# Optimization experiments

Measured on AMD Instinct MI355X. Metric: run time of the kernel, lower is better.

The kernel has to match this reference:

```python
import jax, jax.numpy as jnp
import numpy as np

KEY_DIM = 32
VALUE_DIM = 64
HEADS = 8
CHAN = 256


def conv1x1(x, w, b):
    # x: [b, c, h, w], w: [out, c], b: [out]  (1x1 conv == channel matmul)
    return jnp.einsum('bchw,oc->bohw', x, w) + b[None, :, None, None]


def setup_inputs() -> dict:
    key = jax.random.key(0)
    ks = jax.random.split(key, 9)
    b, c, h, w = 8, CHAN, 128, 128
    qk_dim = KEY_DIM * HEADS   # 256
    v_dim = VALUE_DIM * HEADS  # 512
    s = 0.02
    return {
        'x':  jax.random.normal(ks[0], (b, c, h, w), jnp.float32),
        'Wq': jax.random.normal(ks[1], (qk_dim, c), jnp.float32) * s,
        'bq': jnp.zeros((qk_dim,), jnp.float32),
        'Wk': jax.random.normal(ks[2], (qk_dim, c), jnp.float32) * s,
        'bk': jnp.zeros((qk_dim,), jnp.float32),
        'Wv': jax.random.normal(ks[3], (v_dim, c), jnp.float32) * s,
        'bv': jnp.zeros((v_dim,), jnp.float32),
        'Wo': jax.random.normal(ks[4], (c, v_dim), jnp.float32) * s,
        'bo': jnp.zeros((c,), jnp.float32),
    }


def reference(x, Wq, bq, Wk, bk, Wv, bv, Wo, bo):
    b, c, h, w = x.shape
    n = h * w
    scale = KEY_DIM ** (-0.25)
    # 1x1 conv projections, reshape to [b, heads, d, n]
    q = conv1x1(x, Wq, bq).reshape(b, HEADS, KEY_DIM, n) * scale
    k = conv1x1(x, Wk, bk).reshape(b, HEADS, KEY_DIM, n) * scale
    v = conv1x1(x, Wv, bv).reshape(b, HEADS, VALUE_DIM, n)
    # softmax over sequence positions for keys
    k = jax.nn.softmax(k, axis=-1)
    # norm_queries=True: softmax over key dim for queries
    q = jax.nn.softmax(q, axis=-2)
    # linear attention: context [b,h,d_k,d_v], then output [b,h,d_v,n]
    ctx = jnp.einsum('bhdn,bhen->bhde', k, v)
    out = jnp.einsum('bhdn,bhde->bhen', q, ctx)
    out = out.reshape(b, HEADS * VALUE_DIM, h, w)
    return conv1x1(out, Wo, bo)
```

## Files before the change

### kernel.cpp

```cpp
#include <hip/hip_runtime.h>
#include <hip/hip_bf16.h>
#include <cstddef>


constexpr int   NPIX     = 16384;
constexpr float QK_SCALE = 0.42044820762685725f;

typedef __attribute__((ext_vector_type(8))) short          bf16x8;
typedef __attribute__((ext_vector_type(8))) unsigned short u16x8;
typedef __attribute__((ext_vector_type(4))) float          f32x4;

__device__ __forceinline__ float bf2f(unsigned short v) {
    union { unsigned int u; float f; } c; c.u = ((unsigned int)v) << 16; return c.f;
}
__device__ __forceinline__ unsigned short f2bf(float f) {
    union { __hip_bfloat16 h; unsigned short s; } c; c.h = __float2bfloat16(f); return c.s;
}
__device__ __forceinline__ void gload_lds16(const void* g, void* l) {
    __builtin_amdgcn_global_load_lds(
        (const __attribute__((address_space(1))) unsigned int*)g,
        (__attribute__((address_space(3))) unsigned int*)l, 16, 0, 0);
}

typedef unsigned short lds_row32[32];

__global__ __launch_bounds__(256) void prep(
    const float* __restrict__ Wq, const float* __restrict__ Wk,
    unsigned short* __restrict__ Wqb, unsigned short* __restrict__ Wkb)
{
    const int i = blockIdx.x * 256 + threadIdx.x;
    Wqb[i] = f2bf(Wq[i]);
    Wkb[i] = f2bf(Wk[i]);
}

template<bool QPASS>
__global__ __launch_bounds__(256) void proj_mfma(
    const float* __restrict__ x, const unsigned short* __restrict__ Wb,
    const float* __restrict__ bias, unsigned short* __restrict__ eout,
    float* __restrict__ ksump2)
{
    __shared__ alignas(16) unsigned char smem[36864];
    lds_row32* As1 = (lds_row32*)smem;
    unsigned short (*BsT)[40] = (unsigned short(*)[40])(smem + 16384);
    const int b  = blockIdx.z;
    const int m0 = blockIdx.y * 128;
    const int n0 = blockIdx.x * 128;
    const int t  = threadIdx.x;
    const int w  = t >> 6, l = t & 63;
    const int lm = l & 15, lg = l >> 4;
    const int mwl = (w & 1) * 64;
    const int nwl = (w >> 1) * 64;
    const int lgs = (lg ^ ((lm & 3) ^ ((lm >> 2) & 3))) * 8;
    const int r16 = l >> 2;
    const int scb = ((l & 3) ^ ((r16 & 3) ^ ((r16 >> 2) & 3))) * 8;

    const unsigned short* Abase = Wb + (size_t)m0 * 256;
    const float* xb = x + (size_t)b * 256 * NPIX + n0;
    const int np = (t & 63) * 2, kq = (t >> 6) * 8;

    f32x4 acc[4][4] = {};
    for (int k0 = 0; k0 < 256; k0 += 32) {
        #pragma unroll
        for (int i = 0; i < 2; ++i) {
            const int row0 = w*32 + i*16;
            gload_lds16(Abase + (size_t)(row0 + r16)*256 + k0 + scb, &As1[row0][0]);
        }
        {
            const float* src = xb + (size_t)(k0 + kq) * NPIX + np;
            float2 v[8];
            #pragma unroll
            for (int r = 0; r < 8; ++r)
                v[r] = *(const float2*)(src + (size_t)r * NPIX);
            u16x8 pa, pb;
            #pragma unroll
            for (int r = 0; r < 8; ++r) { pa[r] = f2bf(v[r].x); pb[r] = f2bf(v[r].y); }
            *(u16x8*)&BsT[np][kq]     = pa;
            *(u16x8*)&BsT[np + 1][kq] = pb;
        }
        __syncthreads();
        bf16x8 afr[4], bfr[4];
        #pragma unroll
        for (int i = 0; i < 4; ++i)
            afr[i] = *(const bf16x8*)&As1[mwl + i*16 + lm][lgs];
        #pragma unroll
        for (int j = 0; j < 4; ++j)
            bfr[j] = *(const bf16x8*)&BsT[nwl + j*16 + lm][lg*8];
        #pragma unroll
        for (int i = 0; i < 4; ++i)
            #pragma unroll
            for (int j = 0; j < 4; ++j)
                acc[i][j] = __builtin_amdgcn_mfma_f32_16x16x32_bf16(afr[i], bfr[j], acc[i][j], 0, 0, 0);
        __syncthreads();
    }

    unsigned short (*Cs)[64][72] = (unsigned short(*)[64][72])smem;
    const int mw = m0 + mwl, nw = n0 + nwl;
    float ksloc[4][4];
    #pragma unroll
    for (int i = 0; i < 4; ++i) {
        const f32x4 bb4 = *(const f32x4*)(bias + mw + i*16 + lg*4);
        #pragma unroll
        for (int r = 0; r < 4; ++r) {
            const int row = i*16 + lg*4 + r;
            float cs = 0.f;
            #pragma unroll
            for (int j = 0; j < 4; ++j) {
                const int col = j*16 + lm;
                const unsigned short bs = f2bf(__expf(QK_SCALE * (acc[i][j][r] + bb4[r])));
                if (QPASS) Cs[w][col][row] = bs;
                else { Cs[w][row][col] = bs; cs += bf2f(bs); }
            }
            ksloc[i][r] = cs;
        }
    }
    if (!QPASS) {
        #pragma unroll
        for (int i = 0; i < 4; ++i)
            #pragma unroll
            for (int r = 0; r < 4; ++r) {
                float v = ksloc[i][r];
                v += __shfl_xor(v, 1, 64);
                v += __shfl_xor(v, 2, 64);
                v += __shfl_xor(v, 4, 64);
                v += __shfl_xor(v, 8, 64);
                if (lm == 0) {
                    const int nt2 = blockIdx.x * 2 + (w >> 1);
                    ksump2[((size_t)b*256 + nt2)*256 + mw + i*16 + lg*4 + r] = v;
                }
            }
    }
    __syncthreads();

    if (QPASS) {
        unsigned short* dst = eout + ((size_t)b * NPIX + nw + l) * 256 + mw;
        u16x8 vv[8];
        float z0 = 0.f, z1 = 0.f;
        #pragma unroll
        for (int s8 = 0; s8 < 8; ++s8) {
            vv[s8] = *(const u16x8*)&Cs[w][l][s8*8];
            float ps = 0.f;
            #pragma unroll
            for (int u = 0; u < 8; ++u) ps += bf2f(vv[s8][u]);
            if (s8 < 4) z0 += ps; else z1 += ps;
        }
        const float iz0 = 1.0f / z0, iz1 = 1.0f / z1;
        #pragma unroll
        for (int s8 = 0; s8 < 8; ++s8) {
            const float iz = (s8 < 4) ? iz0 : iz1;
            u16x8 o;
            #pragma unroll
            for (int u = 0; u < 8; ++u) o[u] = f2bf(bf2f(vv[s8][u]) * iz);
            *(u16x8*)(dst + s8*8) = o;
        }
    } else {
        unsigned short* dst = eout + ((size_t)b * 256 + mw + l) * NPIX + nw;
        #pragma unroll
        for (int s8 = 0; s8 < 8; ++s8)
            *(u16x8*)(dst + s8*8) = *(const u16x8*)&Cs[w][l][s8*8];
    }
}

__global__ __launch_bounds__(256) void ksum_red(
    const float* __restrict__ ksump2, float* __restrict__ ksum)
{
    const int t = threadIdx.x;
    const int row = blockIdx.x * 32 + (t >> 3);
    const int b = row >> 8, c = row & 255;
    const int nt0 = t & 7;
    float s = 0.f;
    #pragma unroll 8
    for (int i = 0; i < 32; ++i)
        s += ksump2[((size_t)b*256 + nt0 + 8*i)*256 + c];
    s += __shfl_xor(s, 1, 64);
    s += __shfl_xor(s, 2, 64);
    s += __shfl_xor(s, 4, 64);
    if (nt0 == 0) ksum[row] = s;
}

template<int NCH>
__global__ __launch_bounds__(256) void t_mfma(
    const unsigned short* __restrict__ ek, const float* __restrict__ x,
    float* __restrict__ Tpart)
{
    __shared__ alignas(16) unsigned char smem[32768];
    lds_row32* As = (lds_row32*)smem;
    lds_row32* Bs = (lds_row32*)(smem + 16384);
    const int bid  = blockIdx.x;
    const int v    = bid & 7, s = bid >> 3;
    const int gidx = s >> 2, q = s & 3;
    const int group = v + 8 * gidx;
    const int b = group / NCH, chunk = group % NCH;
    const int mt = (q >> 1) * 128, ct = (q & 1) * 128;
    constexpr int CHPX = NPIX / NCH;

    const int t = threadIdx.x;
    const int w = t >> 6, l = t & 63;
    const int lm = l & 15, lg = l >> 4;
    const int mw = (w & 1) * 64, cw = (w >> 1) * 64;
    const int r16 = l >> 2;
    const int scb = ((l & 3) ^ ((r16 & 3) ^ ((r16 >> 2) & 3))) * 8;
    const int lgs = (lg ^ ((lm & 3) ^ ((lm >> 2) & 3))) * 8;
    const int brq = t >> 3;
    const int bc4 = (t & 7) * 4;
    const int bslot = (t & 7) >> 1;
    const int bhalf = (t & 1) * 4;

    const unsigned short* Abase = ek + ((size_t)b*256 + mt) * NPIX;
    const float*          Bbase = x  + ((size_t)b*256 + ct) * NPIX;
    const int p0base = chunk * CHPX;

    f32x4 breg[4];
    f32x4 acc[4][4] = {};

    #pragma unroll
    for (int i = 0; i < 2; ++i) {
        const int row0 = w*32 + i*16;
        gload_lds16(Abase + (size_t)(row0 + r16) * NPIX + p0base + scb, &As[row0][0]);
    }
    #pragma unroll
    for (int it = 0; it < 4; ++it)
        breg[it] = *(const f32x4*)(Bbase + (size_t)(it*32 + brq) * NPIX + p0base + bc4);
    #pragma unroll
    for (int it = 0; it < 4; ++it) {
        const int row = it*32 + brq;
        const int sl = bslot ^ ((row & 3) ^ ((row >> 2) & 3));
        unsigned short o[4] = { f2bf(breg[it].x), f2bf(breg[it].y),
                                f2bf(breg[it].z), f2bf(breg[it].w) };
        *(ushort4*)&Bs[row][sl*8 + bhalf] = *(ushort4*)o;
    }
    __syncthreads();

    constexpr int ITERS = CHPX / 32;
    for (int t8 = 0; t8 < ITERS; ++t8) {
        const int cur = t8 & 1;
        if (t8 < ITERS - 1) {
            const int p0 = p0base + (t8 + 1) * 32;
            #pragma unroll
            for (int i = 0; i < 2; ++i) {
                const int row0 = w*32 + i*16;
                gload_lds16(Abase + (size_t)(row0 + r16) * NPIX + p0 + scb,
                            &As[(cur^1)*128 + row0][0]);
            }
            #pragma unroll
            for (int it = 0; it < 4; ++it)
                breg[it] = *(const f32x4*)(Bbase + (size_t)(it*32 + brq) * NPIX + p0 + bc4);
        }
        bf16x8 afr[4], bfr[4];
        #pragma unroll
        for (int i = 0; i < 4; ++i)
            afr[i] = *(const bf16x8*)&As[cur*128 + mw + i*16 + lm][lgs];
        #pragma unroll
        for (int j = 0; j < 4; ++j)
            bfr[j] = *(const bf16x8*)&Bs[cur*128 + cw + j*16 + lm][lgs];
        #pragma unroll
        for (int i = 0; i < 4; ++i)
            #pragma unroll
            for (int j = 0; j < 4; ++j)
                acc[i][j] = __builtin_amdgcn_mfma_f32_16x16x32_bf16(afr[i], bfr[j], acc[i][j], 0, 0, 0);
        if (t8 < ITERS - 1) {
            #pragma unroll
            for (int it = 0; it < 4; ++it) {
                const int row = it*32 + brq;
                const int sl = bslot ^ ((row & 3) ^ ((row >> 2) & 3));
                unsigned short o[4] = { f2bf(breg[it].x), f2bf(breg[it].y),
                                        f2bf(breg[it].z), f2bf(breg[it].w) };
                *(ushort4*)&Bs[(cur^1)*128 + row][sl*8 + bhalf] = *(ushort4*)o;
            }
        }
        __syncthreads();
    }

    float* dst = Tpart + ((size_t)(b*NCH + chunk) * 256) * 256;
    #pragma unroll
    for (int i = 0; i < 4; ++i)
        #pragma unroll
        for (int r = 0; r < 4; ++r) {
            const int gm = mt + mw + i*16 + lg*4 + r;
            #pragma unroll
            for (int j = 0; j < 4; ++j)
                dst[(size_t)gm * 256 + ct + cw + j*16 + lm] = acc[i][j][r];
        }
}

template<int NCH>
__global__ __launch_bounds__(256) void treduce(
    float* __restrict__ Tpart, const float* __restrict__ ksum)
{
    const int gid = blockIdx.x * 256 + threadIdx.x;
    const int b   = gid >> 14;
    const int rem = gid & 16383;
    const int r   = rem >> 6;
    const int c4  = (rem & 63) * 4;
    float* base = Tpart + (((size_t)b*NCH) * 256 + r) * 256 + c4;
    f32x4 s = *(f32x4*)base;
    #pragma unroll
    for (int ch = 1; ch < NCH; ++ch) {
        f32x4 v = *(const f32x4*)(base + (size_t)ch * 65536);
        s.x += v.x; s.y += v.y; s.z += v.z; s.w += v.w;
    }
    const float inv = 1.0f / ksum[b*256 + r];
    s.x *= inv; s.y *= inv; s.z *= inv; s.w *= inv;
    *(f32x4*)base = s;
}

template<int NCH>
__global__ __launch_bounds__(256) void ctx_pass(
    const float* __restrict__ Tpart, const float* __restrict__ Wv,
    const float* __restrict__ bv, float* __restrict__ ctx)
{
    const int gid = blockIdx.x * 256 + threadIdx.x;
    const int b   = gid >> 14;
    const int rem = gid & 16383;
    const int h   = rem >> 11;
    const int de  = rem & 2047;
    const int d   = de >> 6;
    const int e   = de & 63;
    const float* tp = Tpart + (((size_t)b*NCH) * 256 + h*32 + d) * 256;
    const float* wv = Wv + (size_t)(h*64 + e) * 256;
    float sx = 0.f, sy = 0.f, sz = 0.f, sw = 0.f;
    #pragma unroll 8
    for (int c = 0; c < 256; c += 4) {
        f32x4 a = *(const f32x4*)(tp + c);
        f32x4 wv4 = *(const f32x4*)(wv + c);
        sx = fmaf(a.x, wv4.x, sx); sy = fmaf(a.y, wv4.y, sy);
        sz = fmaf(a.z, wv4.z, sz); sw = fmaf(a.w, wv4.w, sw);
    }
    ctx[gid] = (sx + sy) + (sz + sw) + bv[h*64 + e];
}

__global__ __launch_bounds__(256) void mpass(
    const float* __restrict__ ctx, const float* __restrict__ Wo,
    unsigned short* __restrict__ Mb)
{
    const int gid = blockIdx.x * 256 + threadIdx.x;
    const int b   = gid >> 16;
    const int rem = gid & 65535;
    const int o   = rem >> 8;
    const int dg  = rem & 255;
    const int h   = dg >> 5;
    const float* cp = ctx + ((size_t)b*8 + h) * 2048 + (dg & 31) * 64;
    const float* wp = Wo + (size_t)o * 512 + h*64;
    float sx = 0.f, sy = 0.f, sz = 0.f, sw = 0.f;
    #pragma unroll
    for (int e = 0; e < 64; e += 4) {
        f32x4 a = *(const f32x4*)(cp + e);
        f32x4 wv = *(const f32x4*)(wp + e);
        sx = fmaf(a.x, wv.x, sx); sy = fmaf(a.y, wv.y, sy);
        sz = fmaf(a.z, wv.z, sz); sw = fmaf(a.w, wv.w, sw);
    }
    Mb[((size_t)b*256 + o) * 256 + dg] = f2bf((sx + sy) + (sz + sw));
}

__global__ __launch_bounds__(256) void out_mfma(
    const unsigned short* __restrict__ eqT, const unsigned short* __restrict__ Mb,
    const float* __restrict__ bo, float* __restrict__ out)
{
    __shared__ alignas(16) unsigned char smem[32768];
    lds_row32* As0 = (lds_row32*)smem;
    lds_row32* Bs0 = (lds_row32*)(smem + 16384);
    const int b  = blockIdx.z;
    const int m0 = blockIdx.y * 128;
    const int n0 = blockIdx.x * 128;
    const int t  = threadIdx.x;
    const int w  = t >> 6, l = t & 63;
    const int lm = l & 15, lg = l >> 4;
    const int mwl = (w & 1) * 64, nwl = (w >> 1) * 64;
    const int lgs = (lg ^ ((lm & 3) ^ ((lm >> 2) & 3))) * 8;
    const int r16 = l >> 2;
    const int scb = ((l & 3) ^ ((r16 & 3) ^ ((r16 >> 2) & 3))) * 8;

    const unsigned short* Abase = Mb  + ((size_t)b*256 + m0) * 256;
    const unsigned short* Bbase = eqT + ((size_t)b*NPIX + n0) * 256;

    auto stage = [&](int buf, int k0) {
        #pragma unroll
        for (int i = 0; i < 2; ++i) {
            const int row0 = w*32 + i*16;
            gload_lds16(Abase + (size_t)(row0 + r16)*256 + k0 + scb, &As0[buf*128 + row0][0]);
            gload_lds16(Bbase + (size_t)(row0 + r16)*256 + k0 + scb, &Bs0[buf*128 + row0][0]);
        }
    };

    f32x4 acc[4][4] = {};
    stage(0, 0);
    __syncthreads();
    for (int t8 = 0; t8 < 8; ++t8) {
        const int cur = t8 & 1;
        if (t8 < 7) stage(cur ^ 1, (t8 + 1) * 32);
        bf16x8 afr[4], bfr[4];
        #pragma unroll
        for (int i = 0; i < 4; ++i)
            afr[i] = *(const bf16x8*)&As0[cur*128 + mwl + i*16 + lm][lgs];
        #pragma unroll
        for (int j = 0; j < 4; ++j)
            bfr[j] = *(const bf16x8*)&Bs0[cur*128 + nwl + j*16 + lm][lgs];
        #pragma unroll
        for (int i = 0; i < 4; ++i)
            #pragma unroll
            for (int j = 0; j < 4; ++j)
                acc[i][j] = __builtin_amdgcn_mfma_f32_16x16x32_bf16(afr[i], bfr[j], acc[i][j], 0, 0, 0);
        __syncthreads();
    }

    #pragma unroll
    for (int i = 0; i < 4; ++i) {
        const f32x4 bb4 = *(const f32x4*)(bo + m0 + mwl + i*16 + lg*4);
        #pragma unroll
        for (int r = 0; r < 4; ++r) {
            const int gm = m0 + mwl + i*16 + lg*4 + r;
            float* dst = out + ((size_t)b*256 + gm) * NPIX + n0 + nwl;
            #pragma unroll
            for (int j = 0; j < 4; ++j)
                dst[j*16 + lm] = acc[i][j][r] + bb4[r];
        }
    }
}

extern "C" void kernel_launch(void* const* d_in, const int* in_sizes, int n_in,
                              void* d_out, int out_size, void* d_ws, size_t ws_size,
                              hipStream_t stream)
{
    const float* x  = (const float*)d_in[0];
    const float* Wq = (const float*)d_in[1];
    const float* bq = (const float*)d_in[2];
    const float* Wk = (const float*)d_in[3];
    const float* bk = (const float*)d_in[4];
    const float* Wv = (const float*)d_in[5];
    const float* bv = (const float*)d_in[6];
    const float* Wo = (const float*)d_in[7];
    const float* bo = (const float*)d_in[8];
    float* out = (float*)d_out;
    char* wsb = (char*)d_ws;

    const bool big = ws_size >= (size_t)102506496;
    if (!big && ws_size < (size_t)89399296) return;

    unsigned short* ekq = (unsigned short*)wsb;
    float *Tpart, *ksump2, *ksum, *ctx;
    unsigned short *Mb, *Wqb, *Wkb;
    if (big) {
        Tpart  = (float*)(wsb + 67108864);
        ksump2 = (float*)(wsb + 67108864);
        ctx    = (float*)(wsb + 100663296);
        ksum   = (float*)(wsb + 101187584);
        Mb     = (unsigned short*)(wsb + 101195776);
        Wqb    = (unsigned short*)(wsb + 102244352);
        Wkb    = (unsigned short*)(wsb + 102375424);
    } else {
        Tpart  = (float*)(wsb + 67108864);
        ksump2 = (float*)(wsb + 67108864);
        ctx    = (float*)(wsb + 83886080);
        ksum   = (float*)(wsb + 84410368);
        Mb     = (unsigned short*)(wsb + 88088576);
        Wqb    = (unsigned short*)(wsb + 89137152);
        Wkb    = (unsigned short*)(wsb + 89268224);
    }

    prep            <<<256,             256, 0, stream>>>(Wq, Wk, Wqb, Wkb);
    proj_mfma<false><<<dim3(128, 2, 8), 256, 0, stream>>>(x, Wkb, bk, ekq, ksump2);
    ksum_red        <<<64,              256, 0, stream>>>(ksump2, ksum);
    if (big) {
        t_mfma<16> <<<512, 256, 0, stream>>>(ekq, x, Tpart);
        treduce<16><<<512, 256, 0, stream>>>(Tpart, ksum);
        ctx_pass<16><<<512, 256, 0, stream>>>(Tpart, Wv, bv, ctx);
    } else {
        t_mfma<8>  <<<256, 256, 0, stream>>>(ekq, x, Tpart);
        treduce<8> <<<512, 256, 0, stream>>>(Tpart, ksum);
        ctx_pass<8><<<512, 256, 0, stream>>>(Tpart, Wv, bv, ctx);
    }
    mpass           <<<2048,            256, 0, stream>>>(ctx, Wo, Mb);
    proj_mfma<true> <<<dim3(128, 2, 8), 256, 0, stream>>>(x, Wqb, bq, ekq, ksump2);
    out_mfma        <<<dim3(128, 2, 8), 256, 0, stream>>>(ekq, Mb, bo, out);
}
```

Before: 253.3 us.

## Double-buffer A and B tiles in projection GEMM to overlap loads with MFMA

The projection kernel's K loop now keeps two LDS buffers for the weight tile and the transposed x tile. While the MFMAs run on the current buffer, it issues the async global-to-LDS weight load and the register prefetch of x for the next buffer, converting x to bf16 and writing it to LDS only after the MFMAs. This hides global-load latency behind compute and removes one barrier per iteration. The cost is higher register pressure from the prefetched x values, and it relies on the existing LDS allocation being large enough for both buffers.

```diff
diff --git a/kernel.cpp b/kernel.cpp
--- a/kernel.cpp
+++ b/kernel.cpp
@@ -40,7 +40,7 @@
     float* __restrict__ ksump2)
 {
     __shared__ alignas(16) unsigned char smem[36864];
-    lds_row32* As1 = (lds_row32*)smem;
+    lds_row32* As = (lds_row32*)smem;
     unsigned short (*BsT)[40] = (unsigned short(*)[40])(smem + 16384);
     const int b  = blockIdx.z;
     const int m0 = blockIdx.y * 128;
@@ -58,38 +58,51 @@
     const float* xb = x + (size_t)b * 256 * NPIX + n0;
     const int np = (t & 63) * 2, kq = (t >> 6) * 8;
 
-    f32x4 acc[4][4] = {};
-    for (int k0 = 0; k0 < 256; k0 += 32) {
+    float2 breg[8];
+    auto stageA = [&](int buf, int k0) {
         #pragma unroll
         for (int i = 0; i < 2; ++i) {
             const int row0 = w*32 + i*16;
-            gload_lds16(Abase + (size_t)(row0 + r16)*256 + k0 + scb, &As1[row0][0]);
-        }
-        {
-            const float* src = xb + (size_t)(k0 + kq) * NPIX + np;
-            float2 v[8];
-            #pragma unroll
-            for (int r = 0; r < 8; ++r)
-                v[r] = *(const float2*)(src + (size_t)r * NPIX);
-            u16x8 pa, pb;
-            #pragma unroll
-            for (int r = 0; r < 8; ++r) { pa[r] = f2bf(v[r].x); pb[r] = f2bf(v[r].y); }
-            *(u16x8*)&BsT[np][kq]     = pa;
-            *(u16x8*)&BsT[np + 1][kq] = pb;
-        }
-        __syncthreads();
+            gload_lds16(Abase + (size_t)(row0 + r16)*256 + k0 + scb,
+                        &As[buf*128 + row0][0]);
+        }
+    };
+    auto loadB = [&](int k0) {
+        const float* src = xb + (size_t)(k0 + kq) * NPIX + np;
+        #pragma unroll
+        for (int r = 0; r < 8; ++r)
+            breg[r] = *(const float2*)(src + (size_t)r * NPIX);
+    };
+    auto writeB = [&](int buf) {
+        u16x8 pa, pb;
+        #pragma unroll
+        for (int r = 0; r < 8; ++r) { pa[r] = f2bf(breg[r].x); pb[r] = f2bf(breg[r].y); }
+        *(u16x8*)&BsT[buf*128 + np][kq]     = pa;
+        *(u16x8*)&BsT[buf*128 + np + 1][kq] = pb;
+    };
+
+    f32x4 acc[4][4] = {};
+    stageA(0, 0); loadB(0); writeB(0);
+    __syncthreads();
+    for (int t8 = 0; t8 < 8; ++t8) {
+        const int cur = t8 & 1;
+        if (t8 < 7) {
+            stageA(cur ^ 1, (t8 + 1) * 32);
+            loadB((t8 + 1) * 32);
+        }
         bf16x8 afr[4], bfr[4];
         #pragma unroll
         for (int i = 0; i < 4; ++i)
-            afr[i] = *(const bf16x8*)&As1[mwl + i*16 + lm][lgs];
+            afr[i] = *(const bf16x8*)&As[cur*128 + mwl + i*16 + lm][lgs];
         #pragma unroll
         for (int j = 0; j < 4; ++j)
-            bfr[j] = *(const bf16x8*)&BsT[nwl + j*16 + lm][lg*8];
+            bfr[j] = *(const bf16x8*)&BsT[cur*128 + nwl + j*16 + lm][lg*8];
         #pragma unroll
         for (int i = 0; i < 4; ++i)
             #pragma unroll
             for (int j = 0; j < 4; ++j)
                 acc[i][j] = __builtin_amdgcn_mfma_f32_16x16x32_bf16(afr[i], bfr[j], acc[i][j], 0, 0, 0);
+        if (t8 < 7) writeB(cur ^ 1);
         __syncthreads();
     }
 
```

Result: slower. 264.5 us (+4.4%).

## Pre-transpose x to bf16 pixel-major and stage both GEMM operands via direct LDS loads

Applied to the files above, without the earlier changes.

Adds a transpose pass that converts x from fp32 channel-major to bf16 pixel-major, using the output buffer as scratch. The Q and K projection kernels then read this layout and stage both operands with 16-byte global-to-LDS loads instead of converting and transposing fp32 x inside each projection. The goal is less fp32 traffic and conversion work, since x is read twice (once for K, once for Q). In exchange it adds an extra kernel that reads all of x and writes a bf16 copy, and it relies on the output buffer being free until out_mfma runs.

```diff
diff --git a/kernel.cpp b/kernel.cpp
--- a/kernel.cpp
+++ b/kernel.cpp
@@ -33,8 +33,152 @@
     Wkb[i] = f2bf(Wk[i]);
 }
 
+__global__ __launch_bounds__(256) void xt_pass(
+    const float* __restrict__ x, unsigned short* __restrict__ xTb)
+{
+    __shared__ float tile[64][65];
+    const int b = blockIdx.z, c0 = blockIdx.y * 64, n0 = blockIdx.x * 64;
+    const int t = threadIdx.x;
+    const int tr = t >> 2, tc = (t & 3) * 16;
+    const float* src = x + ((size_t)b*256 + c0 + tr) * NPIX + n0 + tc;
+    #pragma unroll
+    for (int u = 0; u < 16; u += 4) {
+        f32x4 v = *(const f32x4*)(src + u);
+        tile[tr][tc+u+0] = v.x; tile[tr][tc+u+1] = v.y;
+        tile[tr][tc+u+2] = v.z; tile[tr][tc+u+3] = v.w;
+    }
+    __syncthreads();
+    unsigned short* dst = xTb + ((size_t)b*NPIX + n0 + tr) * 256 + c0 + tc;
+    u16x8 p0, p1;
+    #pragma unroll
+    for (int u = 0; u < 8; ++u) p0[u] = f2bf(tile[tc+u][tr]);
+    #pragma unroll
+    for (int u = 0; u < 8; ++u) p1[u] = f2bf(tile[tc+8+u][tr]);
+    *(u16x8*)dst = p0; *(u16x8*)(dst + 8) = p1;
+}
+
 template<bool QPASS>
-__global__ __launch_bounds__(256) void proj_mfma(
+__global__ __launch_bounds__(256) void proj_xt(
+    const unsigned short* __restrict__ xTb, const unsigned short* __restrict__ Wb,
+    const float* __restrict__ bias, unsigned short* __restrict__ eout,
+    float* __restrict__ ksump2)
+{
+    __shared__ alignas(16) unsigned char smem[36864];
+    lds_row32* As = (lds_row32*)smem;
+    lds_row32* Bs = (lds_row32*)(smem + 16384);
+    const int b  = blockIdx.z;
+    const int m0 = blockIdx.y * 128;
+    const int n0 = blockIdx.x * 128;
+    const int t  = threadIdx.x;
+    const int w  = t >> 6, l = t & 63;
+    const int lm = l & 15, lg = l >> 4;
+    const int mwl = (w & 1) * 64, nwl = (w >> 1) * 64;
+    const int lgs = (lg ^ ((lm & 3) ^ ((lm >> 2) & 3))) * 8;
+    const int r16 = l >> 2;
+    const int scb = ((l & 3) ^ ((r16 & 3) ^ ((r16 >> 2) & 3))) * 8;
+
+    const unsigned short* Abase = Wb + (size_t)m0 * 256;
+    const unsigned short* Bbase = xTb + ((size_t)b*NPIX + n0) * 256;
+
+    auto stage = [&](int buf, int k0) {
+        #pragma unroll
+        for (int i = 0; i < 2; ++i) {
+            const int row0 = w*32 + i*16;
+            gload_lds16(Abase + (size_t)(row0 + r16)*256 + k0 + scb, &As[buf*128 + row0][0]);
+            gload_lds16(Bbase + (size_t)(row0 + r16)*256 + k0 + scb, &Bs[buf*128 + row0][0]);
+        }
+    };
+
+    f32x4 acc[4][4] = {};
+    stage(0, 0);
+    __syncthreads();
+    for (int t8 = 0; t8 < 8; ++t8) {
+        const int cur = t8 & 1;
+        if (t8 < 7) stage(cur ^ 1, (t8 + 1) * 32);
+        bf16x8 afr[4], bfr[4];
+        #pragma unroll
+        for (int i = 0; i < 4; ++i)
+            afr[i] = *(const bf16x8*)&As[cur*128 + mwl + i*16 + lm][lgs];
+        #pragma unroll
+        for (int j = 0; j < 4; ++j)
+            bfr[j] = *(const bf16x8*)&Bs[cur*128 + nwl + j*16 + lm][lgs];
+        #pragma unroll
+        for (int i = 0; i < 4; ++i)
+            #pragma unroll
+            for (int j = 0; j < 4; ++j)
+                acc[i][j] = __builtin_amdgcn_mfma_f32_16x16x32_bf16(afr[i], bfr[j], acc[i][j], 0, 0, 0);
+        __syncthreads();
+    }
+
+    unsigned short (*Cs)[64][72] = (unsigned short(*)[64][72])smem;
+    const int mw = m0 + mwl, nw = n0 + nwl;
+    float ksloc[4][4];
+    #pragma unroll
+    for (int i = 0; i < 4; ++i) {
+        const f32x4 bb4 = *(const f32x4*)(bias + mw + i*16 + lg*4);
+        #pragma unroll
+        for (int r = 0; r < 4; ++r) {
+            const int row = i*16 + lg*4 + r;
+            float cs = 0.f;
+            #pragma unroll
+            for (int j = 0; j < 4; ++j) {
+                const int col = j*16 + lm;
+                const unsigned short bs = f2bf(__expf(QK_SCALE * (acc[i][j][r] + bb4[r])));
+                if (QPASS) Cs[w][col][row] = bs;
+                else { Cs[w][row][col] = bs; cs += bf2f(bs); }
+            }
+            ksloc[i][r] = cs;
+        }
+    }
+    if (!QPASS) {
+        #pragma unroll
+        for (int i = 0; i < 4; ++i)
+            #pragma unroll
+            for (int r = 0; r < 4; ++r) {
+                float v = ksloc[i][r];
+                v += __shfl_xor(v, 1, 64);
+                v += __shfl_xor(v, 2, 64);
+                v += __shfl_xor(v, 4, 64);
+                v += __shfl_xor(v, 8, 64);
+                if (lm == 0) {
+                    const int nt2 = blockIdx.x * 2 + (w >> 1);
+                    ksump2[((size_t)b*256 + nt2)*256 + mw + i*16 + lg*4 + r] = v;
+                }
+            }
+    }
+    __syncthreads();
+
+    if (QPASS) {
+        unsigned short* dst = eout + ((size_t)b * NPIX + nw + l) * 256 + mw;
+        u16x8 vv[8];
+        float z0 = 0.f, z1 = 0.f;
+        #pragma unroll
+        for (int s8 = 0; s8 < 8; ++s8) {
+            vv[s8] = *(const u16x8*)&Cs[w][l][s8*8];
+            float ps = 0.f;
+            #pragma unroll
+            for (int u = 0; u < 8; ++u) ps += bf2f(vv[s8][u]);
+            if (s8 < 4) z0 += ps; else z1 += ps;
+        }
+        const float iz0 = 1.0f / z0, iz1 = 1.0f / z1;
+        #pragma unroll
+        for (int s8 = 0; s8 < 8; ++s8) {
+            const float iz = (s8 < 4) ? iz0 : iz1;
+            u16x8 o;
+            #pragma unroll
+            for (int u = 0; u < 8; ++u) o[u] = f2bf(bf2f(vv[s8][u]) * iz);
+            *(u16x8*)(dst + s8*8) = o;
+        }
+    } else {
+        unsigned short* dst = eout + ((size_t)b * 256 + mw + l) * NPIX + nw;
+        #pragma unroll
+        for (int s8 = 0; s8 < 8; ++s8)
+            *(u16x8*)(dst + s8*8) = *(const u16x8*)&Cs[w][l][s8*8];
+    }
+}
+
+template<bool QPASS>
+__global__ __launch_bounds__(256) void proj_g(
     const float* __restrict__ x, const unsigned short* __restrict__ Wb,
     const float* __restrict__ bias, unsigned short* __restrict__ eout,
     float* __restrict__ ksump2)
@@ -436,6 +580,7 @@
     if (!big && ws_size < (size_t)89399296) return;
 
     unsigned short* ekq = (unsigned short*)wsb;
+    unsigned short* xTb = (unsigned short*)d_out;
     float *Tpart, *ksump2, *ksum, *ctx;
     unsigned short *Mb, *Wqb, *Wkb;
     if (big) {
@@ -456,19 +601,25 @@
         Wkb    = (unsigned short*)(wsb + 89268224);
     }
 
-    prep            <<<256,             256, 0, stream>>>(Wq, Wk, Wqb, Wkb);
-    proj_mfma<false><<<dim3(128, 2, 8), 256, 0, stream>>>(x, Wkb, bk, ekq, ksump2);
-    ksum_red        <<<64,              256, 0, stream>>>(ksump2, ksum);
+    prep<<<256, 256, 0, stream>>>(Wq, Wk, Wqb, Wkb);
     if (big) {
-        t_mfma<16> <<<512, 256, 0, stream>>>(ekq, x, Tpart);
-        treduce<16><<<512, 256, 0, stream>>>(Tpart, ksum);
-        ctx_pass<16><<<512, 256, 0, stream>>>(Tpart, Wv, bv, ctx);
+        xt_pass        <<<dim3(256, 4, 8), 256, 0, stream>>>(x, xTb);
+        proj_xt<false> <<<dim3(128, 2, 8), 256, 0, stream>>>(xTb, Wkb, bk, ekq, ksump2);
+        ksum_red       <<<64,              256, 0, stream>>>(ksump2, ksum);
+        t_mfma<16>     <<<512,             256, 0, stream>>>(ekq, x, Tpart);
+        treduce<16>    <<<512,             256, 0, stream>>>(Tpart, ksum);
+        ctx_pass<16>   <<<512,             256, 0, stream>>>(Tpart, Wv, bv, ctx);
+        mpass          <<<2048,            256, 0, stream>>>(ctx, Wo, Mb);
+        proj_xt<true>  <<<dim3(128, 2, 8), 256, 0, stream>>>(xTb, Wqb, bq, ekq, ksump2);
+        out_mfma       <<<dim3(128, 2, 8), 256, 0, stream>>>(ekq, Mb, bo, out);
     } else {
-        t_mfma<8>  <<<256, 256, 0, stream>>>(ekq, x, Tpart);
-        treduce<8> <<<512, 256, 0, stream>>>(Tpart, ksum);
-        ctx_pass<8><<<512, 256, 0, stream>>>(Tpart, Wv, bv, ctx);
-    }
-    mpass           <<<2048,            256, 0, stream>>>(ctx, Wo, Mb);
-    proj_mfma<true> <<<dim3(128, 2, 8), 256, 0, stream>>>(x, Wqb, bq, ekq, ksump2);
-    out_mfma        <<<dim3(128, 2, 8), 256, 0, stream>>>(ekq, Mb, bo, out);
-}
+        proj_g<false>  <<<dim3(128, 2, 8), 256, 0, stream>>>(x, Wkb, bk, ekq, ksump2);
+        ksum_red       <<<64,              256, 0, stream>>>(ksump2, ksum);
+        t_mfma<8>      <<<256,             256, 0, stream>>>(ekq, x, Tpart);
+        treduce<8>     <<<512,             256, 0, stream>>>(Tpart, ksum);
+        ctx_pass<8>    <<<512,             256, 0, stream>>>(Tpart, Wv, bv, ctx);
+        mpass          <<<2048,            256, 0, stream>>>(ctx, Wo, Mb);
+        proj_g<true>   <<<dim3(128, 2, 8), 256, 0, stream>>>(x, Wqb, bq, ekq, ksump2);
+        out_mfma       <<<dim3(128, 2, 8), 256, 0, stream>>>(ekq, Mb, bo, out);
+    }
+}
```

Result: slower. 284.3 us (+12.2%).

## Fuse K and Q projections into one kernel sharing the x tile

Applied to the files above, without the earlier changes.

Replaces the two separate launches of the projection kernel, one for K and one for Q, with a single kernel. Each block stages the converted x tile once and runs MFMAs against both the Wk and Wq tiles, then writes exp(K) with its partial row sums and the normalised exp(Q)ᵀ to two separate workspace buffers. The goal is to avoid reading and converting the large fp32 input twice. In exchange it doubles the accumulator registers, which may lower occupancy, and it needs a larger workspace. The small-workspace fallback is removed, so the kernel now returns without computing if the workspace is too small.

```diff
diff --git a/kernel.cpp b/kernel.cpp
--- a/kernel.cpp
+++ b/kernel.cpp
@@ -5,6 +5,7 @@
 
 constexpr int   NPIX     = 16384;
 constexpr float QK_SCALE = 0.42044820762685725f;
+constexpr int   NCH      = 16;
 
 typedef __attribute__((ext_vector_type(8))) short          bf16x8;
 typedef __attribute__((ext_vector_type(8))) unsigned short u16x8;
@@ -33,14 +34,15 @@
     Wkb[i] = f2bf(Wk[i]);
 }
 
-template<bool QPASS>
-__global__ __launch_bounds__(256) void proj_mfma(
-    const float* __restrict__ x, const unsigned short* __restrict__ Wb,
-    const float* __restrict__ bias, unsigned short* __restrict__ eout,
+__global__ __launch_bounds__(256, 2) void kq_proj(
+    const float* __restrict__ x,
+    const unsigned short* __restrict__ Wkb, const unsigned short* __restrict__ Wqb,
+    const float* __restrict__ bk, const float* __restrict__ bq,
+    unsigned short* __restrict__ ek, unsigned short* __restrict__ eqT,
     float* __restrict__ ksump2)
 {
     __shared__ alignas(16) unsigned char smem[36864];
-    lds_row32* As1 = (lds_row32*)smem;
+    lds_row32* As = (lds_row32*)smem;
     unsigned short (*BsT)[40] = (unsigned short(*)[40])(smem + 16384);
     const int b  = blockIdx.z;
     const int m0 = blockIdx.y * 128;
@@ -54,16 +56,19 @@
     const int r16 = l >> 2;
     const int scb = ((l & 3) ^ ((r16 & 3) ^ ((r16 >> 2) & 3))) * 8;
 
-    const unsigned short* Abase = Wb + (size_t)m0 * 256;
+    const unsigned short* AbK = Wkb + (size_t)m0 * 256;
+    const unsigned short* AbQ = Wqb + (size_t)m0 * 256;
     const float* xb = x + (size_t)b * 256 * NPIX + n0;
     const int np = (t & 63) * 2, kq = (t >> 6) * 8;
 
-    f32x4 acc[4][4] = {};
+    f32x4 accK[4][4] = {};
+    f32x4 accQ[4][4] = {};
     for (int k0 = 0; k0 < 256; k0 += 32) {
         #pragma unroll
         for (int i = 0; i < 2; ++i) {
             const int row0 = w*32 + i*16;
-            gload_lds16(Abase + (size_t)(row0 + r16)*256 + k0 + scb, &As1[row0][0]);
+            gload_lds16(AbK + (size_t)(row0 + r16)*256 + k0 + scb, &As[row0][0]);
+            gload_lds16(AbQ + (size_t)(row0 + r16)*256 + k0 + scb, &As[128 + row0][0]);
         }
         {
             const float* src = xb + (size_t)(k0 + kq) * NPIX + np;
@@ -78,42 +83,45 @@
             *(u16x8*)&BsT[np + 1][kq] = pb;
         }
         __syncthreads();
-        bf16x8 afr[4], bfr[4];
-        #pragma unroll
-        for (int i = 0; i < 4; ++i)
-            afr[i] = *(const bf16x8*)&As1[mwl + i*16 + lm][lgs];
+        bf16x8 bfr[4];
         #pragma unroll
         for (int j = 0; j < 4; ++j)
             bfr[j] = *(const bf16x8*)&BsT[nwl + j*16 + lm][lg*8];
         #pragma unroll
-        for (int i = 0; i < 4; ++i)
-            #pragma unroll
-            for (int j = 0; j < 4; ++j)
-                acc[i][j] = __builtin_amdgcn_mfma_f32_16x16x32_bf16(afr[i], bfr[j], acc[i][j], 0, 0, 0);
+        for (int i = 0; i < 4; ++i) {
+            bf16x8 ak = *(const bf16x8*)&As[mwl + i*16 + lm][lgs];
+            bf16x8 aq = *(const bf16x8*)&As[128 + mwl + i*16 + lm][lgs];
+            #pragma unroll
+            for (int j = 0; j < 4; ++j) {
+                accK[i][j] = __builtin_amdgcn_mfma_f32_16x16x32_bf16(ak, bfr[j], accK[i][j], 0, 0, 0);
+                accQ[i][j] = __builtin_amdgcn_mfma_f32_16x16x32_bf16(aq, bfr[j], accQ[i][j], 0, 0, 0);
+            }
+        }
         __syncthreads();
     }
 
     unsigned short (*Cs)[64][72] = (unsigned short(*)[64][72])smem;
     const int mw = m0 + mwl, nw = n0 + nwl;
-    float ksloc[4][4];
-    #pragma unroll
-    for (int i = 0; i < 4; ++i) {
-        const f32x4 bb4 = *(const f32x4*)(bias + mw + i*16 + lg*4);
-        #pragma unroll
-        for (int r = 0; r < 4; ++r) {
-            const int row = i*16 + lg*4 + r;
-            float cs = 0.f;
-            #pragma unroll
-            for (int j = 0; j < 4; ++j) {
-                const int col = j*16 + lm;
-                const unsigned short bs = f2bf(__expf(QK_SCALE * (acc[i][j][r] + bb4[r])));
-                if (QPASS) Cs[w][col][row] = bs;
-                else { Cs[w][row][col] = bs; cs += bf2f(bs); }
-            }
-            ksloc[i][r] = cs;
-        }
-    }
-    if (!QPASS) {
+
+    {
+        float ksloc[4][4];
+        #pragma unroll
+        for (int i = 0; i < 4; ++i) {
+            const f32x4 bb4 = *(const f32x4*)(bk + mw + i*16 + lg*4);
+            #pragma unroll
+            for (int r = 0; r < 4; ++r) {
+                const int row = i*16 + lg*4 + r;
+                float cs = 0.f;
+                #pragma unroll
+                for (int j = 0; j < 4; ++j) {
+                    const int col = j*16 + lm;
+                    const unsigned short bs = f2bf(__expf(QK_SCALE * (accK[i][j][r] + bb4[r])));
+                    Cs[w][row][col] = bs;
+                    cs += bf2f(bs);
+                }
+                ksloc[i][r] = cs;
+            }
+        }
         #pragma unroll
         for (int i = 0; i < 4; ++i)
             #pragma unroll
@@ -128,11 +136,30 @@
                     ksump2[((size_t)b*256 + nt2)*256 + mw + i*16 + lg*4 + r] = v;
                 }
             }
-    }
-    __syncthreads();
-
-    if (QPASS) {
-        unsigned short* dst = eout + ((size_t)b * NPIX + nw + l) * 256 + mw;
+        __syncthreads();
+        unsigned short* dst = ek + ((size_t)b * 256 + mw + l) * NPIX + nw;
+        #pragma unroll
+        for (int s8 = 0; s8 < 8; ++s8)
+            *(u16x8*)(dst + s8*8) = *(const u16x8*)&Cs[w][l][s8*8];
+        __syncthreads();
+    }
+
+    {
+        #pragma unroll
+        for (int i = 0; i < 4; ++i) {
+            const f32x4 bb4 = *(const f32x4*)(bq + mw + i*16 + lg*4);
+            #pragma unroll
+            for (int r = 0; r < 4; ++r) {
+                const int row = i*16 + lg*4 + r;
+                #pragma unroll
+                for (int j = 0; j < 4; ++j) {
+                    const int col = j*16 + lm;
+                    Cs[w][col][row] = f2bf(__expf(QK_SCALE * (accQ[i][j][r] + bb4[r])));
+                }
+            }
+        }
+        __syncthreads();
+        unsigned short* dst = eqT + ((size_t)b * NPIX + nw + l) * 256 + mw;
         u16x8 vv[8];
         float z0 = 0.f, z1 = 0.f;
         #pragma unroll
@@ -152,11 +179,6 @@
             for (int u = 0; u < 8; ++u) o[u] = f2bf(bf2f(vv[s8][u]) * iz);
             *(u16x8*)(dst + s8*8) = o;
         }
-    } else {
-        unsigned short* dst = eout + ((size_t)b * 256 + mw + l) * NPIX + nw;
-        #pragma unroll
-        for (int s8 = 0; s8 < 8; ++s8)
-            *(u16x8*)(dst + s8*8) = *(const u16x8*)&Cs[w][l][s8*8];
     }
 }
 
@@ -177,7 +199,6 @@
     if (nt0 == 0) ksum[row] = s;
 }
 
-template<int NCH>
 __global__ __launch_bounds__(256) void t_mfma(
     const unsigned short* __restrict__ ek, const float* __restrict__ x,
     float* __restrict__ Tpart)
@@ -282,7 +303,6 @@
         }
 }
 
-template<int NCH>
 __global__ __launch_bounds__(256) void treduce(
     float* __restrict__ Tpart, const float* __restrict__ ksum)
 {
@@ -303,7 +323,6 @@
     *(f32x4*)base = s;
 }
 
-template<int NCH>
 __global__ __launch_bounds__(256) void ctx_pass(
     const float* __restrict__ Tpart, const float* __restrict__ Wv,
     const float* __restrict__ bv, float* __restrict__ ctx)
@@ -432,43 +451,24 @@
     float* out = (float*)d_out;
     char* wsb = (char*)d_ws;
 
-    const bool big = ws_size >= (size_t)102506496;
-    if (!big && ws_size < (size_t)89399296) return;
-
-    unsigned short* ekq = (unsigned short*)wsb;
-    float *Tpart, *ksump2, *ksum, *ctx;
-    unsigned short *Mb, *Wqb, *Wkb;
-    if (big) {
-        Tpart  = (float*)(wsb + 67108864);
-        ksump2 = (float*)(wsb + 67108864);
-        ctx    = (float*)(wsb + 100663296);
-        ksum   = (float*)(wsb + 101187584);
-        Mb     = (unsigned short*)(wsb + 101195776);
-        Wqb    = (unsigned short*)(wsb + 102244352);
-        Wkb    = (unsigned short*)(wsb + 102375424);
-    } else {
-        Tpart  = (float*)(wsb + 67108864);
-        ksump2 = (float*)(wsb + 67108864);
-        ctx    = (float*)(wsb + 83886080);
-        ksum   = (float*)(wsb + 84410368);
-        Mb     = (unsigned short*)(wsb + 88088576);
-        Wqb    = (unsigned short*)(wsb + 89137152);
-        Wkb    = (unsigned short*)(wsb + 89268224);
-    }
-
-    prep            <<<256,             256, 0, stream>>>(Wq, Wk, Wqb, Wkb);
-    proj_mfma<false><<<dim3(128, 2, 8), 256, 0, stream>>>(x, Wkb, bk, ekq, ksump2);
-    ksum_red        <<<64,              256, 0, stream>>>(ksump2, ksum);
-    if (big) {
-        t_mfma<16> <<<512, 256, 0, stream>>>(ekq, x, Tpart);
-        treduce<16><<<512, 256, 0, stream>>>(Tpart, ksum);
-        ctx_pass<16><<<512, 256, 0, stream>>>(Tpart, Wv, bv, ctx);
-    } else {
-        t_mfma<8>  <<<256, 256, 0, stream>>>(ekq, x, Tpart);
-        treduce<8> <<<512, 256, 0, stream>>>(Tpart, ksum);
-        ctx_pass<8><<<512, 256, 0, stream>>>(Tpart, Wv, bv, ctx);
-    }
-    mpass           <<<2048,            256, 0, stream>>>(ctx, Wo, Mb);
-    proj_mfma<true> <<<dim3(128, 2, 8), 256, 0, stream>>>(x, Wqb, bq, ekq, ksump2);
-    out_mfma        <<<dim3(128, 2, 8), 256, 0, stream>>>(ekq, Mb, bo, out);
-}
+    if (ws_size < (size_t)169615360) return;
+
+    unsigned short* ek    = (unsigned short*)wsb;
+    unsigned short* eqT   = (unsigned short*)(wsb + 67108864);
+    float*          Tpart = (float*)(wsb + 134217728);
+    float*          ksump2= (float*)(wsb + 134217728);
+    float*          ctx   = (float*)(wsb + 167772160);
+    float*          ksum  = (float*)(wsb + 168296448);
+    unsigned short* Mb    = (unsigned short*)(wsb + 168304640);
+    unsigned short* Wqb   = (unsigned short*)(wsb + 169353216);
+    unsigned short* Wkb   = (unsigned short*)(wsb + 169484288);
+
+    prep    <<<256,             256, 0, stream>>>(Wq, Wk, Wqb, Wkb);
+    kq_proj <<<dim3(128, 2, 8), 256, 0, stream>>>(x, Wkb, Wqb, bk, bq, ek, eqT, ksump2);
+    ksum_red<<<64,              256, 0, stream>>>(ksump2, ksum);
+    t_mfma  <<<512,             256, 0, stream>>>(ek, x, Tpart);
+    treduce <<<512,             256, 0, stream>>>(Tpart, ksum);
+    ctx_pass<<<512,             256, 0, stream>>>(Tpart, Wv, bv, ctx);
+    mpass   <<<2048,            256, 0, stream>>>(ctx, Wo, Mb);
+    out_mfma<<<dim3(128, 2, 8), 256, 0, stream>>>(eqT, Mb, bo, out);
+}
```

New measurement: 268.5 us. 1.06x slower.
